# Kernel tuning notes

Measured on AMD Instinct MI355X. Metric: run time of the kernel, lower is better.

## Reference

```python
import jax, jax.numpy as jnp
import numpy as np

# dims
D = 1024; H = 16; DH = D // H; FF = 4096; E = 4; K = 64; M = 256; B = 2; S = 1024
DEPTH = 1.0 + 12.0 / 24.0 * 0.5  # depth_factor for layer_idx=12, num_layers=24
SCALE = 1.0 / np.sqrt(DH)
GATE_DIM = 128


def _heads(t):
    # (B,S,D) -> (B,H,S,DH)
    return t.reshape(t.shape[0], t.shape[1], H, DH).transpose(0, 2, 1, 3)


def _merge(t):
    # (B,H,S,DH) -> (B,S,D)
    return t.transpose(0, 2, 1, 3).reshape(t.shape[0], t.shape[2], D)


def _ln(x, g, b):
    mu = x.mean(-1, keepdims=True)
    var = x.var(-1, keepdims=True)
    return (x - mu) / jnp.sqrt(var + 1e-5) * g + b


def _mha(x, wq, bq, wk, bk, wv, bv, wo, bo):
    q = _heads(x @ wq + bq); k = _heads(x @ wk + bk); v = _heads(x @ wv + bv)
    s = jnp.einsum('bhqd,bhkd->bhqk', q, k) * SCALE
    a = jax.nn.softmax(s, axis=-1)
    return _merge(jnp.einsum('bhqk,bhkd->bhqd', a, v)) @ wo + bo


def _sparse_mha(x, wq, bq, wk, bk, wv, bv, wo, bo):
    # DynamicSparseAttention: keep top-K scores per query, mask the rest
    q = _heads(x @ wq + bq); k = _heads(x @ wk + bk); v = _heads(x @ wv + bv)
    s = jnp.einsum('bhqd,bhkd->bhqk', q, k) * SCALE
    thr = jax.lax.top_k(s, K)[0][..., -1:]             # kth-largest per query
    s = jnp.where(s >= thr, s, -1e9)
    a = jax.nn.softmax(s, axis=-1)
    return _merge(jnp.einsum('bhqk,bhkd->bhqd', a, v)) @ wo + bo


def _performer(x, wq, bq, wk, bk, wv, bv, wo, bo, wf):
    # LearnedPerformerAttention: learned ReLU feature maps, linear attention
    q = _heads(x @ wq + bq); k = _heads(x @ wk + bk); v = _heads(x @ wv + bv)
    pq = jax.nn.relu(jnp.einsum('bhsd,dm->bhsm', q, wf))
    pk = jax.nn.relu(jnp.einsum('bhsd,dm->bhsm', k, wf))
    kv = jnp.einsum('bhsm,bhsd->bhmd', pk, v)          # (B,H,M,DH)
    z = pk.sum(axis=2)                                  # (B,H,M)
    num = jnp.einsum('bhsm,bhmd->bhsd', pq, kv)
    den = jnp.einsum('bhsm,bhm->bhs', pq, z) + 1e-6
    return _merge(num / den[..., None]) @ wo + bo


def setup_inputs() -> dict:
    key = jax.random.key(0)
    ks = iter(jax.random.split(key, 64))

    def w(shape):
        fan_in = shape[-2] if len(shape) > 1 else shape[-1]
        return (jax.random.normal(next(ks), shape, jnp.float32) / np.sqrt(fan_in))

    inp = {'x': jax.random.normal(next(ks), (B, S, D), jnp.float32)}
    # AdaptiveReasoningGate
    inp['arg_w1'] = w((D, GATE_DIM)); inp['arg_b1'] = jnp.zeros(GATE_DIM)
    inp['arg_w2'] = w((GATE_DIM, 2)); inp['arg_b2'] = jnp.zeros(2)
    # MoE attention: router + per-expert MHA
    inp['moe_wr'] = w((D, E)); inp['moe_br'] = jnp.zeros(E)
    for n in ('wq', 'wk', 'wv', 'wo'):
        inp['moe_' + n] = w((E, D, D))
        inp['moe_b' + n[1]] = jnp.zeros((E, D))
    # sparse attention
    for n in ('wq', 'wk', 'wv', 'wo'):
        inp['sp_' + n] = w((D, D)); inp['sp_b' + n[1]] = jnp.zeros(D)
    # performer attention
    for n in ('wq', 'wk', 'wv', 'wo'):
        inp['pf_' + n] = w((D, D)); inp['pf_b' + n[1]] = jnp.zeros(D)
    inp['pf_wf'] = w((DH, M))
    # TAA gate, attention combiner gate
    inp['taa_wg'] = w((D, 2)); inp['taa_bg'] = jnp.zeros(2)
    inp['ag_w'] = w((D, 2)); inp['ag_b'] = jnp.zeros(2)
    # FFN
    inp['ffn_w1'] = w((D, FF)); inp['ffn_b1'] = jnp.zeros(FF)
    inp['ffn_w2'] = w((FF, D)); inp['ffn_b2'] = jnp.zeros(D)
    # norms
    for i in (1, 2, 3):
        inp[f'n{i}_g'] = jnp.ones(D); inp[f'n{i}_b'] = jnp.zeros(D)
    return inp


def _forward(x, arg_w1, arg_b1, arg_w2, arg_b2,
             moe_wr, moe_br, moe_wq, moe_bq, moe_wk, moe_bk, moe_wv, moe_bv, moe_wo, moe_bo,
             sp_wq, sp_bq, sp_wk, sp_bk, sp_wv, sp_bv, sp_wo, sp_bo,
             pf_wq, pf_bq, pf_wk, pf_bk, pf_wv, pf_bv, pf_wo, pf_bo, pf_wf,
             taa_wg, taa_bg, ag_w, ag_b,
             ffn_w1, ffn_b1, ffn_w2, ffn_b2,
             n1_g, n1_b, n2_g, n2_b, n3_g, n3_b):
    avg = x.mean(axis=1)  # (B,D)
    # AdaptiveReasoningGate (attn_weight computed but unused in original forward)
    gw = jax.nn.sigmoid(jax.nn.gelu(avg @ arg_w1 + arg_b1) @ arg_w2 + arg_b2)
    ffn_weight = gw[:, 1][:, None, None]
    # MoE attention: token-level softmax routing over E expert MHAs
    ex_out = jax.vmap(
        lambda wq, bq, wk, bk, wv, bv, wo, bo: _mha(x, wq, bq, wk, bk, wv, bv, wo, bo)
    )(moe_wq, moe_bq, moe_wk, moe_bk, moe_wv, moe_bv, moe_wo, moe_bo)  # (E,B,S,D)
    gates = jax.nn.softmax(x @ moe_wr + moe_br, axis=-1)               # (B,S,E)
    moe_out = jnp.einsum('ebsd,bse->bsd', ex_out, gates)
    # Hybrid thought-aware attention (dropout = identity, eval mode)
    sp = _sparse_mha(x, sp_wq, sp_bq, sp_wk, sp_bk, sp_wv, sp_bv, sp_wo, sp_bo)
    pf = _performer(x, pf_wq, pf_bq, pf_wk, pf_bk, pf_wv, pf_bv, pf_wo, pf_bo, pf_wf)
    tg = jax.nn.softmax(avg @ taa_wg + taa_bg, axis=-1)
    taa_out = tg[:, 0][:, None, None] * sp + tg[:, 1][:, None, None] * pf
    # gated combine of MoE and TAA paths
    ag = jax.nn.softmax(avg @ ag_w + ag_b, axis=-1)
    attn_out = (ag[:, 0][:, None, None] * moe_out + ag[:, 1][:, None, None] * taa_out) * DEPTH
    x1 = _ln(x + attn_out, n1_g, n1_b)
    ffn_out = (jax.nn.gelu(x1 @ ffn_w1 + ffn_b1) @ ffn_w2 + ffn_b2) * ffn_weight * DEPTH
    x2 = _ln(x1 + ffn_out, n2_g, n2_b)
    return _ln(x2, n3_g, n3_b)


def reference(x, arg_w1, arg_b1, arg_w2, arg_b2,
              moe_wr, moe_br, moe_wq, moe_bq, moe_wk, moe_bk, moe_wv, moe_bv, moe_wo, moe_bo,
              sp_wq, sp_bq, sp_wk, sp_bk, sp_wv, sp_bv, sp_wo, sp_bo,
              pf_wq, pf_bq, pf_wk, pf_bk, pf_wv, pf_bv, pf_wo, pf_bo, pf_wf,
              taa_wg, taa_bg, ag_w, ag_b,
              ffn_w1, ffn_b1, ffn_w2, ffn_b2,
              n1_g, n1_b, n2_g, n2_b, n3_g, n3_b):
    return _forward(x, arg_w1, arg_b1, arg_w2, arg_b2,
                    moe_wr, moe_br, moe_wq, moe_bq, moe_wk, moe_bk, moe_wv, moe_bv, moe_wo, moe_bo,
                    sp_wq, sp_bq, sp_wk, sp_bk, sp_wv, sp_bv, sp_wo, sp_bo,
                    pf_wq, pf_bq, pf_wk, pf_bk, pf_wv, pf_bv, pf_wo, pf_bo, pf_wf,
                    taa_wg, taa_bg, ag_w, ag_b,
                    ffn_w1, ffn_b1, ffn_w2, ffn_b2,
                    n1_g, n1_b, n2_g, n2_b, n3_g, n3_b)
```

## Files before the change

### kernel.cpp

```cpp
#include <hip/hip_runtime.h>
#include <hip/hip_bf16.h>
#include <math.h>

#define Bq 2
#define Sq 1024
#define Dq 1024
#define Hq 16
#define DHq 64
#define FFq 4096
#define Eq 4
#define Kq 64
#define Mq 256
#define GATEq 128
#define BSq (Bq*Sq)
#define DEPTHF 1.25f
#define SCALEF 0.125f
#define DD (Dq*Dq)
#define PLANE ((size_t)BSq*Dq)

typedef __hip_bfloat16 bf16;
typedef __attribute__((ext_vector_type(8))) __bf16 bf16x8;
typedef __attribute__((ext_vector_type(4))) float f32x4;

__device__ __forceinline__ float toF(float v){ return v; }
// ... 26 lines not shown
  __syncthreads();
  int c = 0;
  for (int i = threadIdx.x; i < 4096; i += 256) {
    unsigned e = (xw[i] >> 7) & 0xFFu;
    c += (e >= 0x70u && e <= 0x8Fu) ? 1 : 0;
  }
#pragma unroll
  for (int o = 32; o >= 1; o >>= 1) c += __shfl_xor(c, o);
  if ((threadIdx.x & 63) == 0) atomicAdd(&cnt, c);
  __syncthreads();
  if (threadIdx.x == 0) *flag = (cnt > 2048) ? 1 : 0;
}

__global__ __launch_bounds__(256)
void conv_x_kernel(const int* __restrict__ flag, const void* __restrict__ x, bf16* __restrict__ xb)
{
  int f = *flag;
  int i0 = (blockIdx.x*256 + threadIdx.x)*4;
  if (i0 >= BSq*Dq) return;
  if (f) {
    const bf16* s = (const bf16*)x;
#pragma unroll
    for (int k=0;k<4;k++) xb[i0+k] = s[i0+k];
  } else {
    const float* s = (const float*)x;
#pragma unroll
    for (int k=0;k<4;k++) xb[i0+k] = __float2bfloat16(s[i0+k]);
  }
}

template<typename IT>
__device__ void packseg(bf16* dst, const IT* src, int len)
{
  for (int i = threadIdx.x; i < len; i += 256) dst[i] = __float2bfloat16(toF(src[i]));
}
__global__ __launch_bounds__(256)
void pack_bias_kernel(const int* __restrict__ flag, bf16* arena,
    const void* bq, const void* bk, const void* bv, const void* bo,
    const void* sq, const void* sk, const void* sv, const void* so,
    const void* pq, const void* pk, const void* pv, const void* po,
    const void* f1, const void* f2)
{
  int f = *flag;
  if (f) {
    packseg(arena+0,     (const bf16*)bq, 4096); packseg(arena+4096,  (const bf16*)bk, 4096);
    packseg(arena+8192,  (const bf16*)bv, 4096); packseg(arena+12288, (const bf16*)bo, 4096);
    packseg(arena+16384, (const bf16*)sq, 1024); packseg(arena+17408, (const bf16*)sk, 1024);
    packseg(arena+18432, (const bf16*)sv, 1024); packseg(arena+19456, (const bf16*)so, 1024);
    packseg(arena+20480, (const bf16*)pq, 1024); packseg(arena+21504, (const bf16*)pk, 1024);
    packseg(arena+22528, (const bf16*)pv, 1024); packseg(arena+23552, (const bf16*)po, 1024);
    packseg(arena+24576, (const bf16*)f1, 4096); packseg(arena+28672, (const bf16*)f2, 1024);
  } else {
    packseg(arena+0,     (const float*)bq, 4096); packseg(arena+4096,  (const float*)bk, 4096);
    packseg(arena+8192,  (const float*)bv, 4096); packseg(arena+12288, (const float*)bo, 4096);
    packseg(arena+16384, (const float*)sq, 1024); packseg(arena+17408, (const float*)sk, 1024);
    packseg(arena+18432, (const float*)sv, 1024); packseg(arena+19456, (const float*)so, 1024);
    packseg(arena+20480, (const float*)pq, 1024); packseg(arena+21504, (const float*)pk, 1024);
    packseg(arena+22528, (const float*)pv, 1024); packseg(arena+23552, (const float*)po, 1024);
    packseg(arena+24576, (const float*)f1, 4096); packseg(arena+28672, (const float*)f2, 1024);
  }
}

template<typename IT>
__device__ void packwft_body(const IT* __restrict__ wf, bf16* __restrict__ wft)
{
  int i = blockIdx.x*256 + threadIdx.x;
  if (i >= DHq*Mq) return;
  int d = i >> 8, m = i & 255;
  wft[m*DHq + d] = __float2bfloat16(toF(wf[(size_t)d*Mq + m]));
}
__global__ __launch_bounds__(256)
void pack_wft_kernel(const int* __restrict__ flag, const void* wf, bf16* wft)
{
  if (*flag) packwft_body<bf16>((const bf16*)wf, wft);
  else       packwft_body<float>((const float*)wf, wft);
}

template<typename WT>
__device__ void gemm_core(bf16* As, unsigned* Bs,
    const bf16* __restrict__ A, int lda, const WT* __restrict__ W,
    const bf16* __restrict__ barena, int biasOff,
    const float* __restrict__ rowscale, bf16* __restrict__ C,
    float* __restrict__ Cf, int N, int K, int act)
{
  int tid = threadIdx.x;
  int lane = tid & 63, wave = tid >> 6;
  int wr = wave >> 1, wc = wave & 1;
  int bm = blockIdx.x * 128, bn = blockIdx.y * 128;

  int arow1 = wave*16 + (lane>>2);
  int akey = (arow1 >> 1) & 3;
  int acol = ((lane & 3) ^ akey) * 8;
  const bf16* aP1 = A + (size_t)(bm + arow1)*lda + acol;
  const bf16* aP2 = A + (size_t)(bm + arow1 + 64)*lda + acol;

  int kp = tid >> 4, nb8 = (tid & 15)*8;
  const WT* wP = W + (size_t)(2*kp)*N + bn + nb8;

  f32x4 acc[4][4];
#pragma unroll
  for (int i=0;i<4;i++)
#pragma unroll
    for (int j=0;j<4;j++) acc[i][j] = (f32x4){0.f,0.f,0.f,0.f};

  int m = lane & 15, q = lane >> 4;
  int akey2 = (m >> 1) & 3;
  int aq = (q ^ akey2) * 8;

  const int T = K >> 5;
  uint4 rwa, rwb, rwc, rwd;

  async_lds16(aP1, As + wave*512);
  async_lds16(aP2, As + (wave+4)*512);
  aP1 += 32; aP2 += 32;
  if constexpr (sizeof(WT) == 2) {
    rwa = *(const uint4*)wP;
    rwb = *(const uint4*)(wP + N);
  } else {
    const float* f0 = (const float*)wP;
    const float* f1 = (const float*)(wP + N);
    rwa = *(const uint4*)f0; rwb = *(const uint4*)(f0+4);
    rwc = *(const uint4*)f1; rwd = *(const uint4*)(f1+4);
  }
  wP += (size_t)32*N;

  for (int t = 0; t < T; t++) {
    int cur = t & 1;
    unsigned p[8];
    if constexpr (sizeof(WT) == 2) {
      p[0] = (rwa.x & 0xFFFFu) | (rwb.x << 16);  p[1] = (rwa.x >> 16) | (rwb.x & 0xFFFF0000u);
      p[2] = (rwa.y & 0xFFFFu) | (rwb.y << 16);  p[3] = (rwa.y >> 16) | (rwb.y & 0xFFFF0000u);
      p[4] = (rwa.z & 0xFFFFu) | (rwb.z << 16);  p[5] = (rwa.z >> 16) | (rwb.z & 0xFFFF0000u);
      p[6] = (rwa.w & 0xFFFFu) | (rwb.w << 16);  p[7] = (rwa.w >> 16) | (rwb.w & 0xFFFF0000u);
    } else {
      p[0] = (unsigned)bfb(__uint_as_float(rwa.x)) | ((unsigned)bfb(__uint_as_float(rwc.x)) << 16);
      p[1] = (unsigned)bfb(__uint_as_float(rwa.y)) | ((unsigned)bfb(__uint_as_float(rwc.y)) << 16);
      p[2] = (unsigned)bfb(__uint_as_float(rwa.z)) | ((unsigned)bfb(__uint_as_float(rwc.z)) << 16);
      p[3] = (unsigned)bfb(__uint_as_float(rwa.w)) | ((unsigned)bfb(__uint_as_float(rwc.w)) << 16);
      p[4] = (unsigned)bfb(__uint_as_float(rwb.x)) | ((unsigned)bfb(__uint_as_float(rwd.x)) << 16);
      p[5] = (unsigned)bfb(__uint_as_float(rwb.y)) | ((unsigned)bfb(__uint_as_float(rwd.y)) << 16);
      p[6] = (unsigned)bfb(__uint_as_float(rwb.z)) | ((unsigned)bfb(__uint_as_float(rwd.z)) << 16);
      p[7] = (unsigned)bfb(__uint_as_float(rwb.w)) | ((unsigned)bfb(__uint_as_float(rwd.w)) << 16);
    }
    unsigned* bD = Bs + cur*2112 + kp*132 + nb8;
    *(uint4*)(bD)     = make_uint4(p[0],p[1],p[2],p[3]);
    *(uint4*)(bD + 4) = make_uint4(p[4],p[5],p[6],p[7]);
    asm volatile("s_waitcnt vmcnt(0)" ::: "memory");
    __syncthreads();
    if (t + 1 < T) {
      bf16* asn = As + ((t+1)&1)*4096;
      async_lds16(aP1, asn + wave*512);
      async_lds16(aP2, asn + (wave+4)*512);
      aP1 += 32; aP2 += 32;
      if constexpr (sizeof(WT) == 2) {
        rwa = *(const uint4*)wP;
        rwb = *(const uint4*)(wP + N);
      } else {
        const float* f0 = (const float*)wP;
        const float* f1 = (const float*)(wP + N);
        rwa = *(const uint4*)f0; rwb = *(const uint4*)(f0+4);
        rwc = *(const uint4*)f1; rwd = *(const uint4*)(f1+4);
      }
      wP += (size_t)32*N;
    }
    const bf16* asc = As + cur*4096;
    const unsigned* bsc = Bs + cur*2112;
    bf16x8 av[4], bv[4];
#pragma unroll
    for (int i=0;i<4;i++)
      av[i] = *(const bf16x8*)&asc[(wr*64 + i*16 + m)*32 + aq];
#pragma unroll
    for (int j=0;j<4;j++) {
      int n = wc*64 + j*16 + m;
      unsigned b0 = bsc[(q*4+0)*132 + n];
      unsigned b1 = bsc[(q*4+1)*132 + n];
      unsigned b2 = bsc[(q*4+2)*132 + n];
      unsigned b3 = bsc[(q*4+3)*132 + n];
      uint4 bb = make_uint4(b0,b1,b2,b3);
      bv[j] = *(const bf16x8*)&bb;
    }
#pragma unroll
    for (int i=0;i<4;i++)
#pragma unroll
      for (int j=0;j<4;j++)
        acc[i][j] = __builtin_amdgcn_mfma_f32_16x16x32_bf16(av[i], bv[j], acc[i][j], 0, 0, 0);
  }

#pragma unroll
  for (int i=0;i<4;i++) {
    int row0 = bm + wr*64 + i*16 + q*4;
#pragma unroll
    for (int j=0;j<4;j++) {
      int col = bn + wc*64 + j*16 + m;
      float bvv = barena ? toF(barena[biasOff + col]) : 0.f;
#pragma unroll
      for (int r=0;r<4;r++) {
        size_t idx = (size_t)(row0 + r)*N + col;
        if (Cf) {
          Cf[idx] = acc[i][j][r];
        } else {
          float v = acc[i][j][r] + bvv;
          if (act) v = gelu_f(v);
          if (rowscale) v *= rowscale[row0 + r];
          C[idx] = __float2bfloat16(v);
        }
      }
    }
  }
}

__global__ __launch_bounds__(256, 3)
void gemm6_k(const int* __restrict__ flag, const bf16* Abase, long az,
    const void* w0, const void* w1, const void* w2,
    const void* w3, const void* w4, const void* w5,
    long e0, long e1, long e2, long e3, long e4, long e5,
    int b0, int b1, int b2, int b3, int b4, int b5,
    const float* r0, const float* r1, const float* r2,
    const float* r3, const float* r4, const float* r5,
    bf16* c0, bf16* c1, bf16* c2, bf16* c3, bf16* c4, bf16* c5,
    const bf16* barena, int N, int K)
{
  __shared__ bf16 As[2*4096];
  __shared__ unsigned Bs[2*2112];
  int z = blockIdx.z;
  const void* Wp = (z==0)?w0:(z==1)?w1:(z==2)?w2:(z==3)?w3:(z==4)?w4:w5;
  long eo        = (z==0)?e0:(z==1)?e1:(z==2)?e2:(z==3)?e3:(z==4)?e4:e5;
  int bo         = (z==0)?b0:(z==1)?b1:(z==2)?b2:(z==3)?b3:(z==4)?b4:b5;
  const float* rs= (z==0)?r0:(z==1)?r1:(z==2)?r2:(z==3)?r3:(z==4)?r4:r5;
  bf16* C        = (z==0)?c0:(z==1)?c1:(z==2)?c2:(z==3)?c3:(z==4)?c4:c5;
  const bf16* A  = Abase + (size_t)z*az;
  if (*flag) gemm_core<bf16>(As, Bs, A, K, (const bf16*)Wp + eo, barena, bo, rs, C, nullptr, N, K, 0);
  else       gemm_core<float>(As, Bs, A, K, (const float*)Wp + eo, barena, bo, rs, C, nullptr, N, K, 0);
}

__global__ __launch_bounds__(256, 3)
void gemm1_k(const int* __restrict__ flag, const bf16* A, int lda, const void* W,
             const bf16* barena, int biasOff, const float* rowscale,
             bf16* C, float* Cf, long cfz, int N, int K, int act, int kz)
{
  __shared__ bf16 As[2*4096];
  __shared__ unsigned Bs[2*2112];
  int z = blockIdx.z;
  const bf16* Az = A + (size_t)z*kz;
  long wo = (size_t)z*kz*N;
  float* Cfz = Cf ? (Cf + (size_t)z*cfz) : nullptr;
  if (*flag) gemm_core<bf16>(As, Bs, Az, lda, (const bf16*)W + wo, barena, biasOff, rowscale, C, Cfz, N, K, act);
  else       gemm_core<float>(As, Bs, Az, lda, (const float*)W + wo, barena, biasOff, rowscale, C, Cfz, N, K, act);
}

__global__ __launch_bounds__(256)
void combine_ffn2(const float* __restrict__ pf, const bf16* __restrict__ barena,
                  const float* __restrict__ rs, bf16* __restrict__ out)
{
  int i0 = (blockIdx.x*256 + threadIdx.x)*4;
  float4 s0 = *(const float4*)(pf + i0);
  float4 s1 = *(const float4*)(pf + PLANE + i0);
  float4 s2 = *(const float4*)(pf + 2*PLANE + i0);
  float4 s3 = *(const float4*)(pf + 3*PLANE + i0);
  int row = i0 >> 10, col = i0 & 1023;
  float r = rs[row];
  out[i0+0] = __float2bfloat16((s0.x+s1.x+s2.x+s3.x + toF(barena[28672+col+0])) * r);
  out[i0+1] = __float2bfloat16((s0.y+s1.y+s2.y+s3.y + toF(barena[28672+col+1])) * r);
  out[i0+2] = __float2bfloat16((s0.z+s1.z+s2.z+s3.z + toF(barena[28672+col+2])) * r);
  out[i0+3] = __float2bfloat16((s0.w+s1.w+s2.w+s3.w + toF(barena[28672+col+3])) * r);
}

__global__ __launch_bounds__(256)
void vtrans_kernel(const bf16* __restrict__ Vb, long vz, bf16* __restrict__ Vtb, long vtz)
{
  __shared__ bf16 t[64][72];
  const bf16* V = Vb + (size_t)blockIdx.z*vz;
  bf16* Vt = Vtb + (size_t)blockIdx.z*vtz;
  int bh = blockIdx.x;
  int sc_ = blockIdx.y;
  int b = bh >> 4, h = bh & 15;
  int tid = threadIdx.x;
  {
    int s = tid >> 2, dd = (tid & 3) * 16;
    const bf16* src = &V[((size_t)b*Sq + sc_*64 + s)*Dq + h*64 + dd];
    uint4 a0 = *(const uint4*)src;
    uint4 a1 = *(const uint4*)(src + 8);
    *(uint4*)&t[s][dd]     = a0;
    *(uint4*)&t[s][dd + 8] = a1;
  }
  __syncthreads();
  {
    int d = tid >> 2, sp = (tid & 3) * 16;
    unsigned short buf[16];
#pragma unroll
    for (int e = 0; e < 16; e++) {
      bf16 v = t[sp + e][d];
      buf[e] = *(unsigned short*)&v;
    }
    bf16* dst = &Vt[((size_t)bh*DHq + d)*Sq + sc_*64 + sp];
    *(uint4*)dst       = *(uint4*)&buf[0];
    *(uint4*)(dst + 8) = *(uint4*)&buf[8];
  }
}

__global__ __launch_bounds__(256)
void flash_attn_kernel(const bf16* __restrict__ Q, const bf16* __restrict__ K,
                       const bf16* __restrict__ Vt, bf16* __restrict__ O)
{
  int p_ = blockIdx.x;
  int g_ = (p_ & 7)*4 + ((p_ >> 3) & 3);
  int blk = p_ >> 5;
  int h = g_ & 15, b = g_ >> 4;
  int tid = threadIdx.x, lane = tid & 63, wave = tid >> 6;
  int m = lane & 15, q = lane >> 4;
  size_t base = ((size_t)b*Sq)*Dq + (size_t)h*DHq;
  int q0 = blk*64 + wave*16;

  const bf16* qrow = &Q[base + (size_t)(q0 + m)*Dq + q*8];
  bf16x8 bq0 = *(const bf16x8*)qrow;
  bf16x8 bq1 = *(const bf16x8*)(qrow + 32);

  const bf16* krow = K + base + (size_t)m*Dq + q*8;
  const bf16* vrow = Vt + ((size_t)(b*Hq + h)*DHq + m)*Sq + q*8;

  f32x4 oc[4];
#pragma unroll
  for (int dt=0;dt<4;dt++) oc[dt] = (f32x4){0.f,0.f,0.f,0.f};
  float mrun = -1e30f, lrun = 0.f;

  int srcA = m + ((q & 1) << 5);
  int srcB = srcA + 16;
  bool hi = (q >= 2);

  for (int c0 = 0; c0 < Sq; c0 += 32) {
    const bf16* ka = krow + (size_t)c0*Dq;
    bf16x8 a00 = *(const bf16x8*)ka;
    bf16x8 a01 = *(const bf16x8*)(ka + 32);
    const bf16* kb = ka + (size_t)16*Dq;
    bf16x8 a10 = *(const bf16x8*)kb;
    bf16x8 a11 = *(const bf16x8*)(kb + 32);
    f32x4 c0t = (f32x4){0.f,0.f,0.f,0.f};
    c0t = __builtin_amdgcn_mfma_f32_16x16x32_bf16(a00, bq0, c0t, 0, 0, 0);
    c0t = __builtin_amdgcn_mfma_f32_16x16x32_bf16(a01, bq1, c0t, 0, 0, 0);
    f32x4 c1t = (f32x4){0.f,0.f,0.f,0.f};
    c1t = __builtin_amdgcn_mfma_f32_16x16x32_bf16(a10, bq0, c1t, 0, 0, 0);
    c1t = __builtin_amdgcn_mfma_f32_16x16x32_bf16(a11, bq1, c1t, 0, 0, 0);
#pragma unroll
    for (int r=0;r<4;r++) { c0t[r] *= SCALEF; c1t[r] *= SCALEF; }

    float cmax = fmaxf(fmaxf(fmaxf(c0t[0], c0t[1]), fmaxf(c0t[2], c0t[3])),
                       fmaxf(fmaxf(c1t[0], c1t[1]), fmaxf(c1t[2], c1t[3])));
    cmax = fmaxf(cmax, __shfl_xor(cmax, 16));
    cmax = fmaxf(cmax, __shfl_xor(cmax, 32));

    if (__any(cmax > mrun)) {
      float mnew = fmaxf(mrun, cmax);
      float alpha = __expf(mrun - mnew);
#pragma unroll
      for (int dt=0;dt<4;dt++)
#pragma unroll
        for (int r=0;r<4;r++) oc[dt][r] *= alpha;
      lrun *= alpha;
      mrun = mnew;
    }

    float p0[4], p1[4];
#pragma unroll
    for (int r=0;r<4;r++) { p0[r] = __expf(c0t[r] - mrun); p1[r] = __expf(c1t[r] - mrun); }
    lrun += (p0[0]+p0[1]) + (p0[2]+p0[3]) + (p1[0]+p1[1]) + (p1[2]+p1[3]);

    unsigned d00 = (unsigned)bfb(p0[0]) | ((unsigned)bfb(p0[1]) << 16);
    unsigned d01 = (unsigned)bfb(p0[2]) | ((unsigned)bfb(p0[3]) << 16);
    unsigned d10 = (unsigned)bfb(p1[0]) | ((unsigned)bfb(p1[1]) << 16);
    unsigned d11 = (unsigned)bfb(p1[2]) | ((unsigned)bfb(p1[3]) << 16);
    unsigned X0 = __shfl(d00, srcA, 64);
    unsigned X1 = __shfl(d01, srcA, 64);
    unsigned X2 = __shfl(d00, srcB, 64);
    unsigned X3 = __shfl(d01, srcB, 64);
    unsigned Y0 = __shfl(d10, srcA, 64);
    unsigned Y1 = __shfl(d11, srcA, 64);
    unsigned Y2 = __shfl(d10, srcB, 64);
    unsigned Y3 = __shfl(d11, srcB, 64);
    uint4 bb = make_uint4(hi ? Y0 : X0, hi ? Y1 : X1, hi ? Y2 : X2, hi ? Y3 : X3);
    bf16x8 pb = *(const bf16x8*)&bb;

    const bf16* va = vrow + c0;
#pragma unroll
    for (int dt=0;dt<4;dt++) {
      bf16x8 av = *(const bf16x8*)&va[(size_t)(dt*16)*Sq];
      oc[dt] = __builtin_amdgcn_mfma_f32_16x16x32_bf16(av, pb, oc[dt], 0, 0, 0);
    }
  }

  lrun += __shfl_xor(lrun, 16);
  lrun += __shfl_xor(lrun, 32);
  lrun = fmaxf(lrun, 1e-30f);
  float inv = 1.0f / lrun;
  bf16* orow = O + base + (size_t)(q0 + m)*Dq + q*4;
#pragma unroll
  for (int dt=0;dt<4;dt++) {
    unsigned w0 = (unsigned)bfb(oc[dt][0]*inv) | ((unsigned)bfb(oc[dt][1]*inv) << 16);
    unsigned w1 = (unsigned)bfb(oc[dt][2]*inv) | ((unsigned)bfb(oc[dt][3]*inv) << 16);
    *(uint2*)&orow[dt*16] = make_uint2(w0, w1);
  }
}

template<int SPARSE>
__global__ __launch_bounds__(256, 4)
void attn_kernel(const bf16* __restrict__ Q, const bf16* __restrict__ K,
                 const bf16* __restrict__ Vt, bf16* __restrict__ O)
{
  const int PAST = 1032;
  __shared__ bf16 pa[16*PAST];
  __shared__ float partA[64], partB[64];
  __shared__ int cntb[2][64];

  int p_ = blockIdx.x;
  int g_ = (p_ & 7)*4 + ((p_ >> 3) & 3);
  int rb = p_ >> 5;
  int h  = g_ & 15;
  int b  = g_ >> 4;
  int tid = threadIdx.x, lane = tid & 63, wave = tid >> 6;
  int m = lane & 15, q = lane >> 4;
  size_t base = ((size_t)b*Sq)*Dq + (size_t)h*DHq;
  int q0 = rb*16;

  const bf16* qrow = &Q[base + (size_t)(q0+m)*Dq + q*8];
  bf16x8 aq0 = *(const bf16x8*)qrow;
  bf16x8 aq1 = *(const bf16x8*)(qrow + 32);

  f32x4 cc[16];
#pragma unroll
  for (int t = 0; t < 16; t++) {
    int j0 = wave*256 + t*16;
    const bf16* kp = &K[base + (size_t)(j0+m)*Dq + q*8];
    bf16x8 b0 = *(const bf16x8*)kp;
    bf16x8 b1 = *(const bf16x8*)(kp + 32);
    f32x4 c = {0.f,0.f,0.f,0.f};
    c = __builtin_amdgcn_mfma_f32_16x16x32_bf16(aq0, b0, c, 0, 0, 0);
    c = __builtin_amdgcn_mfma_f32_16x16x32_bf16(aq1, b1, c, 0, 0, 0);
#pragma unroll
    for (int r=0;r<4;r++) c[r] *= SCALEF;
    cc[t] = c;
  }

  unsigned lo[4] = {0u,0u,0u,0u};
  if (SPARSE) {
    int cnt_cur[4] = {Sq, Sq, Sq, Sq};
    for (int bit = 31; bit >= 0; bit--) {
      int par = bit & 1;
      unsigned cand[4];
      float candf[4];
      int c4[4] = {0,0,0,0};
#pragma unroll
      for (int r=0;r<4;r++) {
        cand[r] = lo[r] | (1u << bit);
        candf[r] = thr_decode(cand[r]);
      }
#pragma unroll
      for (int t=0;t<16;t++)
#pragma unroll
        for (int r=0;r<4;r++) c4[r] += (cc[t][r] >= candf[r]) ? 1 : 0;
#pragma unroll
      for (int o=1;o<16;o<<=1)
#pragma unroll
        for (int r=0;r<4;r++) c4[r] += __shfl_xor(c4[r], o);
      if (m == 0) {
#pragma unroll
        for (int r=0;r<4;r++) cntb[par][wave*16 + q*4 + r] = c4[r];
      }
      __syncthreads();
      int done = 1;
#pragma unroll
      for (int r=0;r<4;r++) {
        int row = q*4 + r;
        int tot = cntb[par][row] + cntb[par][16+row] + cntb[par][32+row] + cntb[par][48+row];
        if (tot >= Kq) { lo[r] = cand[r]; cnt_cur[r] = tot; }
        done &= (cnt_cur[r] == Kq) ? 1 : 0;
      }
      done &= __shfl_xor(done, 16);
      done &= __shfl_xor(done, 32);
      if (done) break;
    }
  }

  float mrow[4];
#pragma unroll
  for (int r=0;r<4;r++) {
    float v = -1e30f;
#pragma unroll
    for (int t=0;t<16;t++) v = fmaxf(v, cc[t][r]);
#pragma unroll
    for (int o=1;o<16;o<<=1) v = fmaxf(v, __shfl_xor(v, o));
    mrow[r] = v;
  }
  if (m == 0) {
#pragma unroll
    for (int r=0;r<4;r++) partA[wave*16 + q*4 + r] = mrow[r];
  }
  __syncthreads();
#pragma unroll
  for (int r=0;r<4;r++) {
    int row = q*4 + r;
    mrow[r] = fmaxf(fmaxf(partA[row], partA[16+row]), fmaxf(partA[32+row], partA[48+row]));
  }

  float thrf[4];
  if (SPARSE) {
#pragma unroll
    for (int r=0;r<4;r++) {
      thrf[r] = (!(lo[r] & 0x80000000u) && lo[r] <= 0x007FFFFFu)
                    ? -INFINITY : thr_decode(lo[r]);
    }
  }
  float rsum[4] = {0.f,0.f,0.f,0.f};
#pragma unroll
  for (int t=0;t<16;t++) {
    int col = wave*256 + t*16 + m;
#pragma unroll
    for (int r=0;r<4;r++) {
      float p;
      if (SPARSE) p = (cc[t][r] >= thrf[r]) ? __expf(cc[t][r] - mrow[r]) : 0.f;
      else        p = __expf(cc[t][r] - mrow[r]);
      rsum[r] += p;
      pa[(q*4+r)*PAST + col] = __float2bfloat16(p);
    }
  }
#pragma unroll
  for (int r=0;r<4;r++)
#pragma unroll
    for (int o=1;o<16;o<<=1) rsum[r] += __shfl_xor(rsum[r], o);
  if (m == 0) {
#pragma unroll
    for (int r=0;r<4;r++) partB[wave*16 + q*4 + r] = rsum[r];
  }
  __syncthreads();
#pragma unroll
  for (int r=0;r<4;r++) {
    int row = q*4 + r;
    rsum[r] = partB[row] + partB[16+row] + partB[32+row] + partB[48+row];
    rsum[r] = fmaxf(rsum[r], 1e-30f);
  }

  const bf16* vtp = &Vt[((size_t)(b*Hq + h)*DHq + wave*16 + m)*Sq];
  f32x4 oc = {0.f,0.f,0.f,0.f};
#pragma unroll 8
  for (int ks = 0; ks < 32; ks++) {
    bf16x8 af = *(const bf16x8*)&pa[m*PAST + ks*32 + q*8];
    bf16x8 bv = *(const bf16x8*)&vtp[ks*32 + q*8];
    oc = __builtin_amdgcn_mfma_f32_16x16x32_bf16(af, bv, oc, 0, 0, 0);
  }
#pragma unroll
  for (int r=0;r<4;r++) {
    O[base + (size_t)(q0 + q*4 + r)*Dq + wave*16 + m] = __float2bfloat16(oc[r] / rsum[r]);
  }
}

__global__ __launch_bounds__(256)
void perf_kv_mfma(const bf16* __restrict__ Kb, const bf16* __restrict__ Vt,
                  const bf16* __restrict__ wft, bf16* __restrict__ kvb,
                  float* __restrict__ zg)
{
  __shared__ bf16 pbuf[4][32*40];
  __shared__ float kvred[4][64*32];
  __shared__ float zred[4][32];

  int bh = blockIdx.x;
  int mg = blockIdx.y;
  int b = bh >> 4, h = bh & 15;
  int tid = threadIdx.x, lane = tid & 63, wave = tid >> 6;
  int ml = lane & 15, q = lane >> 4;
  size_t kbase = ((size_t)b*Sq)*Dq + (size_t)h*DHq;
  const bf16* vtb = Vt + (size_t)bh*DHq*Sq;
  int sw0 = wave*256;
  bf16* pw = pbuf[wave];

  bf16x8 awf[2][2];
#pragma unroll
  for (int t=0;t<2;t++) {
    const bf16* p = &wft[(size_t)(mg*32 + t*16 + ml)*DHq + q*8];
    awf[t][0] = *(const bf16x8*)p;
    awf[t][1] = *(const bf16x8*)(p + 32);
  }

  f32x4 acc[4][2];
#pragma unroll
  for (int dt=0;dt<4;dt++)
#pragma unroll
    for (int t=0;t<2;t++) acc[dt][t] = (f32x4){0.f,0.f,0.f,0.f};
  float zacc[2][4] = {{0.f,0.f,0.f,0.f},{0.f,0.f,0.f,0.f}};

  for (int st = 0; st < 8; st++) {
    int s0 = sw0 + st*32;
    f32x4 pk[2][2];
#pragma unroll
    for (int sc=0;sc<2;sc++) {
      const bf16* kp = &Kb[kbase + (size_t)(s0 + sc*16 + ml)*Dq + q*8];
      bf16x8 b0 = *(const bf16x8*)kp;
      bf16x8 b1 = *(const bf16x8*)(kp + 32);
#pragma unroll
      for (int t=0;t<2;t++) {
        f32x4 c = (f32x4){0.f,0.f,0.f,0.f};
        c = __builtin_amdgcn_mfma_f32_16x16x32_bf16(awf[t][0], b0, c, 0, 0, 0);
        c = __builtin_amdgcn_mfma_f32_16x16x32_bf16(awf[t][1], b1, c, 0, 0, 0);
        pk[t][sc] = c;
      }
    }
#pragma unroll
    for (int t=0;t<2;t++)
#pragma unroll
      for (int sc=0;sc<2;sc++)
#pragma unroll
        for (int r=0;r<4;r++) {
          float v = fmaxf(pk[t][sc][r], 0.f);
          zacc[t][r] += v;
          pw[(t*16 + q*4 + r)*40 + sc*16 + ml] = __float2bfloat16(v);
        }
#pragma unroll
    for (int dt=0;dt<4;dt++) {
      bf16x8 av = *(const bf16x8*)&vtb[(size_t)(dt*16 + ml)*Sq + s0 + q*8];
#pragma unroll
      for (int t=0;t<2;t++) {
        bf16x8 bp = *(const bf16x8*)&pw[(t*16 + ml)*40 + q*8];
        acc[dt][t] = __builtin_amdgcn_mfma_f32_16x16x32_bf16(av, bp, acc[dt][t], 0, 0, 0);
      }
    }
  }

#pragma unroll
  for (int dt=0;dt<4;dt++)
#pragma unroll
    for (int t=0;t<2;t++)
#pragma unroll
      for (int r=0;r<4;r++)
        kvred[wave][(dt*16 + q*4 + r)*32 + t*16 + ml] = acc[dt][t][r];
#pragma unroll
  for (int t=0;t<2;t++)
#pragma unroll
    for (int r=0;r<4;r++) {
      float v = zacc[t][r];
#pragma unroll
      for (int o=1;o<16;o<<=1) v += __shfl_xor(v, o);
      if (ml == 0) zred[wave][t*16 + q*4 + r] = v;
    }
  __syncthreads();
  for (int p = tid; p < 2048; p += 256) {
    float s = kvred[0][p] + kvred[1][p] + kvred[2][p] + kvred[3][p];
    int d = p >> 5, mloc = p & 31;
    kvb[(size_t)bh*(DHq*Mq) + d*Mq + mg*32 + mloc] = __float2bfloat16(s);
  }
  if (tid < 32) {
    float s = zred[0][tid] + zred[1][tid] + zred[2][tid] + zred[3][tid];
    zg[bh*Mq + mg*32 + tid] = s;
  }
}

__global__ __launch_bounds__(256)
void perf_out_mfma(const bf16* __restrict__ Q, const bf16* __restrict__ wft,
                   const bf16* __restrict__ kvb, const float* __restrict__ zg,
                   bf16* __restrict__ O)
{
  const int PQST = 264;
  __shared__ bf16 pa2[64*PQST];
  __shared__ float zs[Mq];

  int blk = blockIdx.x;
  int sc_ = blk & 15;
  int bh  = blk >> 4;
  int b = bh >> 4, h = bh & 15;
  int tid = threadIdx.x, lane = tid & 63, wave = tid >> 6;
  int ml = lane & 15, q = lane >> 4;
  size_t base = ((size_t)b*Sq)*Dq + (size_t)h*DHq;
  int s0 = sc_*64;

  zs[tid] = zg[bh*Mq + tid];

  const bf16* qp = &Q[base + (size_t)(s0 + wave*16 + ml)*Dq + q*8];
  bf16x8 aq0 = *(const bf16x8*)qp;
  bf16x8 aq1 = *(const bf16x8*)(qp + 32);
  __syncthreads();

  f32x4 pq[16];
#pragma unroll
  for (int mt=0;mt<16;mt++) {
    const bf16* wp = &wft[(size_t)(mt*16 + ml)*DHq + q*8];
    bf16x8 b0 = *(const bf16x8*)wp;
    bf16x8 b1 = *(const bf16x8*)(wp + 32);
    f32x4 c = (f32x4){0.f,0.f,0.f,0.f};
    c = __builtin_amdgcn_mfma_f32_16x16x32_bf16(aq0, b0, c, 0, 0, 0);
    c = __builtin_amdgcn_mfma_f32_16x16x32_bf16(aq1, b1, c, 0, 0, 0);
    pq[mt] = c;
  }

  float den[4] = {1e-6f, 1e-6f, 1e-6f, 1e-6f};
#pragma unroll
  for (int mt=0;mt<16;mt++)
#pragma unroll
    for (int r=0;r<4;r++) {
      float v = fmaxf(pq[mt][r], 0.f);
      den[r] += v * zs[mt*16 + ml];
      pa2[(wave*16 + q*4 + r)*PQST + mt*16 + ml] = __float2bfloat16(v);
    }
#pragma unroll
  for (int r=0;r<4;r++)
#pragma unroll
    for (int o=1;o<16;o<<=1) den[r] += __shfl_xor(den[r], o);
  __syncthreads();
// ... 12 lines not shown
    }
  }
#pragma unroll
  for (int dt=0;dt<4;dt++)
#pragma unroll
    for (int r=0;r<4;r++)
      O[base + (size_t)(s0 + wave*16 + q*4 + r)*Dq + dt*16 + ml] =
          __float2bfloat16(oc[dt][r] / den[r]);
}

template<typename IT>
__device__ void ln_body(float* buf, float* red, const IT* __restrict__ xb,
                        const void* Ap, const void* Bp,
                        const IT* __restrict__ g, const IT* __restrict__ be,
                        void* out, int mode)
{
  int row = blockIdx.x;
  int tid = threadIdx.x;
  size_t off = (size_t)row*Dq;
  for (int dd = tid; dd < Dq; dd += 256) {
    float v;
    if (mode == 0)      v = toF(xb[off+dd]) + toF(((const bf16*)Ap)[off+dd]);
    else if (mode == 1) v = toF(((const bf16*)Ap)[off+dd]) + toF(((const bf16*)Bp)[off+dd]);
    else if (mode == 3) {
      const bf16* P = (const bf16*)Ap;
      v = toF(xb[off+dd]);
#pragma unroll
      for (int p=0;p<6;p++) v += toF(P[(size_t)p*PLANE + off + dd]);
    }
    else                v = toF(((const bf16*)Ap)[off+dd]);
    buf[dd] = v;
  }
  __syncthreads();
  float s = 0.f, q = 0.f;
  for (int dd = tid; dd < Dq; dd += 256) { float v = buf[dd]; s += v; q += v*v; }
#pragma unroll
  for (int o=32;o>=1;o>>=1) { s += __shfl_xor(s,o); q += __shfl_xor(q,o); }
  int w = tid >> 6;
  if ((tid & 63) == 0) { red[w] = s; red[4+w] = q; }
  __syncthreads();
  if (tid == 0) {
    float S1 = red[0]+red[1]+red[2]+red[3];
    float Q1 = red[4]+red[5]+red[6]+red[7];
    float mu = S1 / (float)Dq;
    float var = Q1 / (float)Dq - mu*mu;
    red[8] = mu; red[9] = rsqrtf(fmaxf(var, 0.f) + 1e-5f);
  }
  __syncthreads();
  float mu = red[8], inv = red[9];
  for (int dd = tid; dd < Dq; dd += 256) {
    float v = (buf[dd]-mu)*inv*toF(g[dd]) + toF(be[dd]);
    if (mode == 2) stF((IT*)out, off+dd, v);
    else           stF((bf16*)out, off+dd, v);
  }
}

__global__ __launch_bounds__(256)
void ln_kernel(const int* __restrict__ flag, const void* xb, const void* A, const void* Bv,
               const void* g, const void* be, void* out, int mode)
{
  __shared__ float buf[Dq];
  __shared__ float red[10];
  if (*flag) ln_body<bf16>(buf, red, (const bf16*)xb, A, Bv, (const bf16*)g, (const bf16*)be, out, mode);
  else       ln_body<float>(buf, red, (const float*)xb, A, Bv, (const float*)g, (const float*)be, out, mode);
}

__global__ __launch_bounds__(256)
void avg2_kernel(const int* __restrict__ flag, const void* __restrict__ x, float* __restrict__ avgsum)
{
  int b  = blockIdx.x >> 4;
  int sc = blockIdx.x & 15;
  int t = threadIdx.x;
  int c0 = t*4;
  float a0=0.f,a1=0.f,a2=0.f,a3=0.f;
  if (*flag) {
    const unsigned* X = (const unsigned*)x;
    for (int s = sc*64; s < sc*64+64; s++) {
      size_t bi = (((size_t)(b*Sq + s))*Dq + c0) >> 1;
      unsigned u0 = X[bi], u1 = X[bi+1];
      a0 += __uint_as_float(u0 << 16);
      a1 += __uint_as_float(u0 & 0xFFFF0000u);
      a2 += __uint_as_float(u1 << 16);
      a3 += __uint_as_float(u1 & 0xFFFF0000u);
    }
  } else {
    const float* X = (const float*)x;
    for (int s = sc*64; s < sc*64+64; s++) {
      float4 v = *(const float4*)&X[((size_t)(b*Sq + s))*Dq + c0];
      a0 += v.x; a1 += v.y; a2 += v.z; a3 += v.w;
    }
  }
  atomicAdd(&avgsum[b*Dq + c0 + 0], a0);
  atomicAdd(&avgsum[b*Dq + c0 + 1], a1);
  atomicAdd(&avgsum[b*Dq + c0 + 2], a2);
  atomicAdd(&avgsum[b*Dq + c0 + 3], a3);
}

template<typename IT>
__device__ void gdots_body(const float* __restrict__ avgs,
    const IT* __restrict__ w1, const IT* __restrict__ b1,
    const IT* __restrict__ taw, const IT* __restrict__ tab,
    const IT* __restrict__ agw, const IT* __restrict__ agb,
    float* __restrict__ g1b, float* __restrict__ lgb)
{
  int blk = blockIdx.x;
  int tid = threadIdx.x, lane = tid & 63, wave = tid >> 6;
  if (blk < 64) {
    int o = blk*4 + wave;
    int bb = o >> 7, j = o & 127;
    const float* av = avgs + bb*Dq;
    float a = 0.f;
#pragma unroll
    for (int k = 0; k < 16; k++) {
      int dd = k*64 + lane;
      a += av[dd] * toF(w1[dd*GATEq + j]);
    }
#pragma unroll
    for (int off=32; off>=1; off>>=1) a += __shfl_xor(a, off);
    if (lane == 0) g1b[o] = gelu_f(a*(1.f/(float)Sq) + toF(b1[j]));
  } else {
    int bb = wave >> 1, c = wave & 1;
    const float* av = avgs + bb*Dq;
    const IT* wm = (blk == 64) ? taw : agw;
    const IT* bm = (blk == 64) ? tab : agb;
    float a = 0.f;
#pragma unroll
    for (int k = 0; k < 16; k++) {
      int dd = k*64 + lane;
      a += av[dd] * toF(wm[dd*2 + c]);
    }
#pragma unroll
    for (int off=32; off>=1; off>>=1) a += __shfl_xor(a, off);
    if (lane == 0) lgb[(blk-64)*4 + wave] = a*(1.f/(float)Sq) + toF(bm[c]);
  }
}
__global__ __launch_bounds__(256)
void gate_dots_kernel(const int* __restrict__ flag, const float* avgs,
    const void* w1, const void* b1, const void* taw, const void* tab,
    const void* agw, const void* agb, float* g1b, float* lgb)
{
  if (*flag) gdots_body<bf16>(avgs, (const bf16*)w1,(const bf16*)b1,(const bf16*)taw,
      (const bf16*)tab,(const bf16*)agw,(const bf16*)agb, g1b, lgb);
  else gdots_body<float>(avgs, (const float*)w1,(const float*)b1,(const float*)taw,
      (const float*)tab,(const float*)agw,(const float*)agb, g1b, lgb);
}

template<typename IT>
__device__ void gfin_body(float* sh, const float* __restrict__ g1b, const float* __restrict__ lgb,
    const IT* __restrict__ w2, const IT* __restrict__ b2,
    float* __restrict__ cmb0, float* __restrict__ rs_tg0,
    float* __restrict__ rs_tg1, float* __restrict__ rs_ffn)
{
  int tid = threadIdx.x, lane = tid & 63, wave = tid >> 6;
  if (wave < 2) {
    float a = g1b[wave*128 + lane] * toF(w2[lane*2 + 1])
            + g1b[wave*128 + 64 + lane] * toF(w2[(64+lane)*2 + 1]);
#pragma unroll
    for (int off=32; off>=1; off>>=1) a += __shfl_xor(a, off);
    if (lane == 0) sh[wave] = 1.f/(1.f + __expf(-(a + toF(b2[1]))));
  }
  __syncthreads();
  if (tid < Bq) {
    int b = tid;
    float t0 = lgb[b*2], t1 = lgb[b*2+1];
    float m = fmaxf(t0,t1);
    float e0=__expf(t0-m), e1=__expf(t1-m), inv=1.f/(e0+e1);
    float tg0 = e0*inv, tg1 = e1*inv;
    float a0 = lgb[4+b*2], a1l = lgb[4+b*2+1];
    m = fmaxf(a0,a1l);
    float f0=__expf(a0-m), f1=__expf(a1l-m); inv = 1.f/(f0+f1);
    float ag0 = f0*inv, ag1 = f1*inv;
    cmb0[b] = ag0*DEPTHF;
    sh[2+b] = tg0*ag1*DEPTHF;
    sh[4+b] = tg1*ag1*DEPTHF;
    sh[6+b] = sh[b]*DEPTHF;
  }
  __syncthreads();
  for (int i = tid; i < BSq; i += 256) {
    int b = i >> 10;
    rs_tg0[i] = sh[2+b]; rs_tg1[i] = sh[4+b]; rs_ffn[i] = sh[6+b];
  }
}
__global__ __launch_bounds__(256)
void gate_fin_kernel(const int* __restrict__ flag, const float* g1b, const float* lgb,
    const void* w2, const void* b2, float* cmb0,
    float* rs_tg0, float* rs_tg1, float* rs_ffn)
{
  __shared__ float sh[8];
  if (*flag) gfin_body<bf16>(sh, g1b, lgb, (const bf16*)w2, (const bf16*)b2, cmb0, rs_tg0, rs_tg1, rs_ffn);
  else       gfin_body<float>(sh, g1b, lgb, (const float*)w2, (const float*)b2, cmb0, rs_tg0, rs_tg1, rs_ffn);
}

template<typename IT>
__device__ void router_body(const IT* __restrict__ x, const IT* __restrict__ wr,
                            const IT* __restrict__ br, const float* __restrict__ cmb0,
                            float* __restrict__ gates_t)
{
  int row = blockIdx.x;
  int tid = threadIdx.x;
  size_t off = (size_t)row*Dq;
  float a0=0,a1=0,a2=0,a3=0;
  for (int dd = tid; dd < Dq; dd += 64) {
    float xv = toF(x[off+dd]);
    a0 += xv*toF(wr[dd*Eq+0]);
    a1 += xv*toF(wr[dd*Eq+1]);
    a2 += xv*toF(wr[dd*Eq+2]);
    a3 += xv*toF(wr[dd*Eq+3]);
  }
#pragma unroll
  for (int o=32;o>=1;o>>=1) {
    a0 += __shfl_xor(a0,o); a1 += __shfl_xor(a1,o);
    a2 += __shfl_xor(a2,o); a3 += __shfl_xor(a3,o);
  }
  if (tid == 0) {
    a0 += toF(br[0]); a1 += toF(br[1]); a2 += toF(br[2]); a3 += toF(br[3]);
    float m = fmaxf(fmaxf(a0,a1),fmaxf(a2,a3));
    float e0=__expf(a0-m), e1=__expf(a1-m), e2=__expf(a2-m), e3=__expf(a3-m);
    float inv = 1.f/(e0+e1+e2+e3);
    float sc = cmb0[row >> 10];
    gates_t[0*BSq+row]=e0*inv*sc; gates_t[1*BSq+row]=e1*inv*sc;
    gates_t[2*BSq+row]=e2*inv*sc; gates_t[3*BSq+row]=e3*inv*sc;
  }
}
__global__ __launch_bounds__(64)
void router_kernel(const int* __restrict__ flag, const void* x, const void* wr,
                   const void* br, const float* cmb0, float* gates_t)
{
  if (*flag) router_body<bf16>((const bf16*)x, (const bf16*)wr, (const bf16*)br, cmb0, gates_t);
  else       router_body<float>((const float*)x, (const float*)wr, (const float*)br, cmb0, gates_t);
}

extern "C" void kernel_launch(void* const* d_in, const int* in_sizes, int n_in,
                              void* d_out, int out_size, void* d_ws, size_t ws_size,
                              hipStream_t stream) {
  const void* x      = d_in[0];
  const void* arg_w1 = d_in[1];  const void* arg_b1 = d_in[2];
  const void* arg_w2 = d_in[3];  const void* arg_b2 = d_in[4];
  const void* moe_wr = d_in[5];  const void* moe_br = d_in[6];
  const void* moe_wq = d_in[7];  const void* moe_bq = d_in[8];
  const void* moe_wk = d_in[9];  const void* moe_bk = d_in[10];
  const void* moe_wv = d_in[11]; const void* moe_bv = d_in[12];
  const void* moe_wo = d_in[13]; const void* moe_bo = d_in[14];
  const void* sp_wq  = d_in[15]; const void* sp_bq  = d_in[16];
  const void* sp_wk  = d_in[17]; const void* sp_bk  = d_in[18];
  const void* sp_wv  = d_in[19]; const void* sp_bv  = d_in[20];
  const void* sp_wo  = d_in[21]; const void* sp_bo  = d_in[22];
  const void* pf_wq  = d_in[23]; const void* pf_bq  = d_in[24];
  const void* pf_wk  = d_in[25]; const void* pf_bk  = d_in[26];
  const void* pf_wv  = d_in[27]; const void* pf_bv  = d_in[28];
  const void* pf_wo  = d_in[29]; const void* pf_bo  = d_in[30];
  const void* pf_wf  = d_in[31];
  const void* taa_wg = d_in[32]; const void* taa_bg = d_in[33];
  const void* ag_w   = d_in[34]; const void* ag_b   = d_in[35];
  const void* ffn_w1 = d_in[36]; const void* ffn_b1 = d_in[37];
  const void* ffn_w2 = d_in[38]; const void* ffn_b2 = d_in[39];
  const void* n1_g   = d_in[40]; const void* n1_b   = d_in[41];
  const void* n2_g   = d_in[42]; const void* n2_b   = d_in[43];
  const void* n3_g   = d_in[44]; const void* n3_b   = d_in[45];

  char* w = (char*)d_ws;
  const size_t MB = 1024*1024;
  bf16* xb  = (bf16*)w;
  bf16* Qp  = (bf16*)(w + 4*MB);
  bf16* KV  = (bf16*)(w + 28*MB);
  bf16* Vt  = (bf16*)(w + 44*MB);
  bf16* Pp  = (bf16*)(w + 28*MB);
  bf16* x1    = (bf16*)(w + 4*MB);
  bf16* ffn_h = (bf16*)(w + 8*MB);
  float* partF= (float*)(w + 24*MB);
  bf16* tmpb  = (bf16*)w;
  bf16* x2    = (bf16*)w;
  char* book = w + 56*MB;
  float* rs_tg0 = (float*)book;
  float* rs_tg1 = rs_tg0 + BSq;
  float* rs_ffn = rs_tg1 + BSq;
  float* cmb0   = rs_ffn + BSq;
  float* avgp   = cmb0 + 16;
  float* gates_t= avgp + Bq*Dq;
  float* zb     = gates_t + Eq*BSq;
  float* g1b    = zb + Bq*Hq*Mq;
  float* lgb    = g1b + 256;
  int*   dflag  = (int*)(lgb + 8);
  bf16*  barena = (bf16*)(dflag + 16);
  bf16*  wft    = barena + 29696;
  bf16*  kvb    = (bf16*)(w + 57*MB);

  detect_kernel<<<1, 256, 0, stream>>>((const unsigned*)x, dflag);
  hipMemsetAsync(avgp, 0, (size_t)(Bq*Dq)*sizeof(float), stream);
  conv_x_kernel<<<BSq*Dq/1024, 256, 0, stream>>>(dflag, x, xb);
  pack_bias_kernel<<<1, 256, 0, stream>>>(dflag, barena,
      moe_bq, moe_bk, moe_bv, moe_bo, sp_bq, sp_bk, sp_bv, sp_bo,
      pf_bq, pf_bk, pf_bv, pf_bo, ffn_b1, ffn_b2);
  pack_wft_kernel<<<64, 256, 0, stream>>>(dflag, pf_wf, wft);
  avg2_kernel<<<Bq*16, 256, 0, stream>>>(dflag, x, avgp);
  gate_dots_kernel<<<66, 256, 0, stream>>>(dflag, avgp, arg_w1, arg_b1,
      taa_wg, taa_bg, ag_w, ag_b, g1b, lgb);
  gate_fin_kernel<<<1, 256, 0, stream>>>(dflag, g1b, lgb, arg_w2, arg_b2,
      cmb0, rs_tg0, rs_tg1, rs_ffn);
  router_kernel<<<BSq, 64, 0, stream>>>(dflag, x, moe_wr, moe_br, cmb0, gates_t);

  dim3 g6(16, 8, 6);
  dim3 gVT(Bq*Hq, Sq/64, 2);
  int nAttnBlk = Bq*Hq*(Sq/16);
  int nFlashBlk = Bq*Hq*(Sq/64);

  for (int p = 0; p < 2; p++) {
    int e0 = 2*p, e1 = 2*p + 1;
    gemm6_k<<<g6, 256, 0, stream>>>(dflag, xb, 0L,
        moe_wq, moe_wk, moe_wv, moe_wq, moe_wk, moe_wv,
        (long)e0*DD, (long)e0*DD, (long)e0*DD, (long)e1*DD, (long)e1*DD, (long)e1*DD,
        e0*1024, e0*1024+4096, e0*1024+8192, e1*1024, e1*1024+4096, e1*1024+8192,
        nullptr, nullptr, nullptr, nullptr, nullptr, nullptr,
        Qp + (size_t)e0*PLANE, KV, KV + PLANE,
        Qp + (size_t)e1*PLANE, KV + 2*PLANE, KV + 3*PLANE,
        barena, Dq, Dq);
    vtrans_kernel<<<gVT, 256, 0, stream>>>(KV + PLANE, (long)(2*PLANE), Vt, (long)PLANE);
    flash_attn_kernel<<<nFlashBlk, 256, 0, stream>>>(Qp + (size_t)e0*PLANE, KV, Vt, Qp + (size_t)e0*PLANE);
    flash_attn_kernel<<<nFlashBlk, 256, 0, stream>>>(Qp + (size_t)e1*PLANE, KV + 2*PLANE, Vt + PLANE, Qp + (size_t)e1*PLANE);
  }

  gemm6_k<<<g6, 256, 0, stream>>>(dflag, xb, 0L,
      sp_wq, sp_wk, sp_wv, pf_wq, pf_wk, pf_wv,
      0L, 0L, 0L, 0L, 0L, 0L,
      16384, 17408, 18432, 20480, 21504, 22528,
      nullptr, nullptr, nullptr, nullptr, nullptr, nullptr,
      Qp + 4*PLANE, KV, KV + PLANE,
      Qp + 5*PLANE, KV + 2*PLANE, KV + 3*PLANE,
      barena, Dq, Dq);
  vtrans_kernel<<<gVT, 256, 0, stream>>>(KV + PLANE, (long)(2*PLANE), Vt, (long)PLANE);
  attn_kernel<1><<<nAttnBlk, 256, 0, stream>>>(Qp + 4*PLANE, KV, Vt, Qp + 4*PLANE);
  {
    dim3 gKV1(Bq*Hq, 8);
    perf_kv_mfma<<<gKV1, 256, 0, stream>>>(KV + 2*PLANE, Vt + PLANE, wft, kvb, zb);
  }
  perf_out_mfma<<<Bq*Hq*16, 256, 0, stream>>>(Qp + 5*PLANE, wft, kvb, zb, Qp + 5*PLANE);

  gemm6_k<<<g6, 256, 0, stream>>>(dflag, Qp, (long)PLANE,
      moe_wo, moe_wo, moe_wo, moe_wo, sp_wo, pf_wo,
      0L, (long)DD, (long)2*DD, (long)3*DD, 0L, 0L,
      12288, 13312, 14336, 15360, 19456, 23552,
      gates_t, gates_t + BSq, gates_t + 2*BSq, gates_t + 3*BSq, rs_tg0, rs_tg1,
      Pp, Pp + PLANE, Pp + 2*PLANE, Pp + 3*PLANE, Pp + 4*PLANE, Pp + 5*PLANE,
      barena, Dq, Dq);

  ln_kernel<<<BSq, 256, 0, stream>>>(dflag, x, Pp, nullptr, n1_g, n1_b, x1, 3);

  gemm1_k<<<dim3(16, 32, 1), 256, 0, stream>>>(dflag, x1, Dq, ffn_w1,
      barena, 24576, nullptr, ffn_h, nullptr, 0L, FFq, Dq, 1, 0);
  gemm1_k<<<dim3(16, 8, 4), 256, 0, stream>>>(dflag, ffn_h, FFq, ffn_w2,
      nullptr, 0, nullptr, nullptr, partF, (long)PLANE, Dq, 1024, 0, 1024);
  combine_ffn2<<<BSq*Dq/1024, 256, 0, stream>>>(partF, barena, rs_ffn, tmpb);

  ln_kernel<<<BSq, 256, 0, stream>>>(dflag, nullptr, x1, tmpb, n2_g, n2_b, x2, 1);
  ln_kernel<<<BSq, 256, 0, stream>>>(dflag, nullptr, x2, nullptr, n3_g, n3_b, d_out, 2);
}
```

Before: 1.093 ms.

## Split flash attention keys across waves with LDS merge and K prefetch

Each flash-attention block now handles 16 queries, and its four waves each process a quarter of the key sequence (split-K). The per-wave partial outputs, maxima and sums are merged through shared memory with a log-sum-exp rescale. The grid grows fourfold, which raises parallelism and shortens each wave's serial loop. K fragments are prefetched one iteration ahead and the V loads are hoisted earlier. The cost is extra shared-memory traffic, a block barrier, and each wave reloading the same Q rows.

```diff
diff --git a/kernel.cpp b/kernel.cpp
--- a/kernel.cpp
+++ b/kernel.cpp
@@ -352,21 +352,25 @@
 void flash_attn_kernel(const bf16* __restrict__ Q, const bf16* __restrict__ K,
                        const bf16* __restrict__ Vt, bf16* __restrict__ O)
 {
+  __shared__ float ocs[4][16][68];
+  __shared__ float mls[4][2][16];
+
   int p_ = blockIdx.x;
   int g_ = (p_ & 7)*4 + ((p_ >> 3) & 3);
-  int blk = p_ >> 5;
+  int qt = p_ >> 5;
   int h = g_ & 15, b = g_ >> 4;
   int tid = threadIdx.x, lane = tid & 63, wave = tid >> 6;
   int m = lane & 15, q = lane >> 4;
   size_t base = ((size_t)b*Sq)*Dq + (size_t)h*DHq;
-  int q0 = blk*64 + wave*16;
+  int q0 = qt*16;
 
   const bf16* qrow = &Q[base + (size_t)(q0 + m)*Dq + q*8];
   bf16x8 bq0 = *(const bf16x8*)qrow;
   bf16x8 bq1 = *(const bf16x8*)(qrow + 32);
 
-  const bf16* krow = K + base + (size_t)m*Dq + q*8;
-  const bf16* vrow = Vt + ((size_t)(b*Hq + h)*DHq + m)*Sq + q*8;
+  int s00 = wave*256;
+  const bf16* krow = K + base + (size_t)(s00 + m)*Dq + q*8;
+  const bf16* vrow = Vt + ((size_t)(b*Hq + h)*DHq + m)*Sq + s00 + q*8;
 
   f32x4 oc[4];
 #pragma unroll
@@ -377,19 +381,31 @@
   int srcB = srcA + 16;
   bool hi = (q >= 2);
 
-  for (int c0 = 0; c0 < Sq; c0 += 32) {
-    const bf16* ka = krow + (size_t)c0*Dq;
-    bf16x8 a00 = *(const bf16x8*)ka;
-    bf16x8 a01 = *(const bf16x8*)(ka + 32);
-    const bf16* kb = ka + (size_t)16*Dq;
-    bf16x8 a10 = *(const bf16x8*)kb;
-    bf16x8 a11 = *(const bf16x8*)(kb + 32);
+  bf16x8 ka00 = *(const bf16x8*)krow;
+  bf16x8 ka01 = *(const bf16x8*)(krow + 32);
+  bf16x8 ka10 = *(const bf16x8*)(krow + (size_t)16*Dq);
+  bf16x8 ka11 = *(const bf16x8*)(krow + (size_t)16*Dq + 32);
+
+  for (int c = 0; c < 8; c++) {
+    bf16x8 kn00, kn01, kn10, kn11;
+    if (c < 7) {
+      const bf16* kn = krow + (size_t)(c+1)*32*Dq;
+      kn00 = *(const bf16x8*)kn;
+      kn01 = *(const bf16x8*)(kn + 32);
+      kn10 = *(const bf16x8*)(kn + (size_t)16*Dq);
+      kn11 = *(const bf16x8*)(kn + (size_t)16*Dq + 32);
+    }
     f32x4 c0t = (f32x4){0.f,0.f,0.f,0.f};
-    c0t = __builtin_amdgcn_mfma_f32_16x16x32_bf16(a00, bq0, c0t, 0, 0, 0);
-    c0t = __builtin_amdgcn_mfma_f32_16x16x32_bf16(a01, bq1, c0t, 0, 0, 0);
+    c0t = __builtin_amdgcn_mfma_f32_16x16x32_bf16(ka00, bq0, c0t, 0, 0, 0);
+    c0t = __builtin_amdgcn_mfma_f32_16x16x32_bf16(ka01, bq1, c0t, 0, 0, 0);
     f32x4 c1t = (f32x4){0.f,0.f,0.f,0.f};
-    c1t = __builtin_amdgcn_mfma_f32_16x16x32_bf16(a10, bq0, c1t, 0, 0, 0);
-    c1t = __builtin_amdgcn_mfma_f32_16x16x32_bf16(a11, bq1, c1t, 0, 0, 0);
+    c1t = __builtin_amdgcn_mfma_f32_16x16x32_bf16(ka10, bq0, c1t, 0, 0, 0);
+    c1t = __builtin_amdgcn_mfma_f32_16x16x32_bf16(ka11, bq1, c1t, 0, 0, 0);
+    const bf16* va = vrow + c*32;
+    bf16x8 av0 = *(const bf16x8*)va;
+    bf16x8 av1 = *(const bf16x8*)&va[(size_t)16*Sq];
+    bf16x8 av2 = *(const bf16x8*)&va[(size_t)32*Sq];
+    bf16x8 av3 = *(const bf16x8*)&va[(size_t)48*Sq];
 #pragma unroll
     for (int r=0;r<4;r++) { c0t[r] *= SCALEF; c1t[r] *= SCALEF; }
 
@@ -429,25 +445,41 @@
     uint4 bb = make_uint4(hi ? Y0 : X0, hi ? Y1 : X1, hi ? Y2 : X2, hi ? Y3 : X3);
     bf16x8 pb = *(const bf16x8*)&bb;
 
-    const bf16* va = vrow + c0;
-#pragma unroll
-    for (int dt=0;dt<4;dt++) {
-      bf16x8 av = *(const bf16x8*)&va[(size_t)(dt*16)*Sq];
-      oc[dt] = __builtin_amdgcn_mfma_f32_16x16x32_bf16(av, pb, oc[dt], 0, 0, 0);
-    }
+    oc[0] = __builtin_amdgcn_mfma_f32_16x16x32_bf16(av0, pb, oc[0], 0, 0, 0);
+    oc[1] = __builtin_amdgcn_mfma_f32_16x16x32_bf16(av1, pb, oc[1], 0, 0, 0);
+    oc[2] = __builtin_amdgcn_mfma_f32_16x16x32_bf16(av2, pb, oc[2], 0, 0, 0);
+    oc[3] = __builtin_amdgcn_mfma_f32_16x16x32_bf16(av3, pb, oc[3], 0, 0, 0);
+
+    if (c < 7) { ka00 = kn00; ka01 = kn01; ka10 = kn10; ka11 = kn11; }
   }
 
   lrun += __shfl_xor(lrun, 16);
   lrun += __shfl_xor(lrun, 32);
-  lrun = fmaxf(lrun, 1e-30f);
-  float inv = 1.0f / lrun;
-  bf16* orow = O + base + (size_t)(q0 + m)*Dq + q*4;
-#pragma unroll
-  for (int dt=0;dt<4;dt++) {
-    unsigned w0 = (unsigned)bfb(oc[dt][0]*inv) | ((unsigned)bfb(oc[dt][1]*inv) << 16);
-    unsigned w1 = (unsigned)bfb(oc[dt][2]*inv) | ((unsigned)bfb(oc[dt][3]*inv) << 16);
-    *(uint2*)&orow[dt*16] = make_uint2(w0, w1);
-  }
+#pragma unroll
+  for (int dt=0;dt<4;dt++)
+    *(float4*)&ocs[wave][m][dt*16 + q*4] = (float4){oc[dt][0], oc[dt][1], oc[dt][2], oc[dt][3]};
+  if (q == 0) { mls[wave][0][m] = mrun; mls[wave][1][m] = lrun; }
+  __syncthreads();
+
+  int mm = tid >> 4, d0 = (tid & 15) * 4;
+  float m0 = mls[0][0][mm], m1 = mls[1][0][mm], m2 = mls[2][0][mm], m3 = mls[3][0][mm];
+  float M = fmaxf(fmaxf(m0, m1), fmaxf(m2, m3));
+  float a0 = __expf(m0 - M), a1 = __expf(m1 - M), a2 = __expf(m2 - M), a3 = __expf(m3 - M);
+  float l = mls[0][1][mm]*a0 + mls[1][1][mm]*a1 + mls[2][1][mm]*a2 + mls[3][1][mm]*a3;
+  l = fmaxf(l, 1e-30f);
+  float inv = 1.0f / l;
+  float4 o0 = *(const float4*)&ocs[0][mm][d0];
+  float4 o1 = *(const float4*)&ocs[1][mm][d0];
+  float4 o2 = *(const float4*)&ocs[2][mm][d0];
+  float4 o3 = *(const float4*)&ocs[3][mm][d0];
+  float r0 = (o0.x*a0 + o1.x*a1 + o2.x*a2 + o3.x*a3) * inv;
+  float r1 = (o0.y*a0 + o1.y*a1 + o2.y*a2 + o3.y*a3) * inv;
+  float r2 = (o0.z*a0 + o1.z*a1 + o2.z*a2 + o3.z*a3) * inv;
+  float r3 = (o0.w*a0 + o1.w*a1 + o2.w*a2 + o3.w*a3) * inv;
+  bf16* op = O + base + (size_t)(q0 + mm)*Dq + d0;
+  unsigned w0 = (unsigned)bfb(r0) | ((unsigned)bfb(r1) << 16);
+  unsigned w1 = (unsigned)bfb(r2) | ((unsigned)bfb(r3) << 16);
+  *(uint2*)op = make_uint2(w0, w1);
 }
 
 template<int SPARSE>
@@ -1066,7 +1098,7 @@
   dim3 g6(16, 8, 6);
   dim3 gVT(Bq*Hq, Sq/64, 2);
   int nAttnBlk = Bq*Hq*(Sq/16);
-  int nFlashBlk = Bq*Hq*(Sq/64);
+  int nFlashBlk = Bq*Hq*(Sq/16);
 
   for (int p = 0; p < 2; p++) {
     int e0 = 2*p, e1 = 2*p + 1;
```

Measured after the change: 1.092 ms. No clear change (-0.1%).
